# Performance work log

Measured on AMD Instinct MI355X. Metric: run time of the kernel, lower is better.

Reference implementation:

```python
import jax, jax.numpy as jnp
import numpy as np
from jax.scipy.special import logsumexp

NUM_TAGS = 128
B, S = 256, 1024


def setup_inputs() -> dict:
    key = jax.random.key(0)
    k1, k2, k3, k4, k5 = jax.random.split(key, 5)
    emissions = jax.random.normal(k1, (B, S, NUM_TAGS), dtype=jnp.float32)
    masks = jnp.ones((B, S), dtype=jnp.float32)
    tags = jax.random.randint(k2, (B, S), 0, NUM_TAGS, dtype=jnp.int64)
    transitions = jax.random.normal(k3, (NUM_TAGS, NUM_TAGS), dtype=jnp.float32)
    start_transitions = jax.random.normal(k4, (NUM_TAGS,), dtype=jnp.float32)
    end_transitions = jax.random.normal(k5, (NUM_TAGS,), dtype=jnp.float32)
    return {"emissions": emissions, "masks": masks, "tags": tags,
            "transitions": transitions, "start_transitions": start_transitions,
            "end_transitions": end_transitions}


def _crf_loss(emissions, masks, tags, transitions, start_transitions, end_transitions):
    b, s, t = emissions.shape

    # ---- forward algorithm (log partition) ----
    def step(alpha, xs):
        emit, m = xs  # emit: (B,T), m: (B,)
        # next[b,j] = logsumexp_i(alpha[b,i] + trans[i,j] + emit[b,j])
        nxt = logsumexp(alpha[:, :, None] + transitions[None, :, :] + emit[:, None, :], axis=1)
        alpha = jnp.where(m[:, None] > 0, nxt, alpha)
        return alpha, None

    alpha0 = jnp.broadcast_to(start_transitions[None, :], (b, t))
    # note: original torch code includes i=0 in the recurrence (applies transitions
    # from start_transitions into the first emission) -- replicated faithfully.
    alpha, _ = jax.lax.scan(step, alpha0,
                            (jnp.swapaxes(emissions, 0, 1), masks.T))
    log_z = logsumexp(alpha + end_transitions[None, :], axis=1)  # (B,)

    # ---- gold sequence score (vectorized over time) ----
    bidx = jnp.arange(b)
    score = start_transitions[tags[:, 0]]
    emit_g = jnp.take_along_axis(emissions, tags[:, :, None], axis=2)[..., 0]  # (B,S)
    score = score + jnp.sum(emit_g[:, : s - 1] * masks[:, : s - 1], axis=1)
    trans_g = transitions[tags[:, : s - 1], tags[:, 1:]]  # (B,S-1)
    score = score + jnp.sum(trans_g * masks[:, 1:], axis=1)
    last_ix = jnp.maximum(jnp.sum(masks, axis=1) - 1.0, 0.0).astype(jnp.int32)
    score = score + emissions[bidx, last_ix, tags[:, -1]] * masks[:, -1]
    score = score + end_transitions[tags[:, -1]] * masks[:, -1]

    return jnp.mean(log_z - score)


def reference(emissions, masks, tags, transitions, start_transitions, end_transitions):
    return _crf_loss(emissions, masks, tags, transitions, start_transitions, end_transitions)
```

## Files before the change

### kernel.cpp

```cpp
#include <hip/hip_runtime.h>

#define NT 128
#define SEQ 1024
#define NB 256

typedef _Float16 half2v __attribute__((ext_vector_type(2)));

#define DPP_MAX_STEP(x, ctrl)                                                   \
    fmaxf((x), __builtin_bit_cast(float, __builtin_amdgcn_update_dpp(           \
        __builtin_bit_cast(int, (x)), __builtin_bit_cast(int, (x)),             \
        (ctrl), 0xf, 0xf, false)))

__device__ __forceinline__ float wave_max_dpp(float x) {
    x = DPP_MAX_STEP(x, 0x111);
    x = DPP_MAX_STEP(x, 0x112);
    x = DPP_MAX_STEP(x, 0x114);
    x = DPP_MAX_STEP(x, 0x118);
    x = DPP_MAX_STEP(x, 0x142);
    x = DPP_MAX_STEP(x, 0x143);
    return __builtin_bit_cast(float, __builtin_amdgcn_readlane(
        __builtin_bit_cast(int, x), 63));
}

__device__ __forceinline__ float cross32_add(float x) {
    float a = x, b = x;
    asm volatile("v_permlane32_swap_b32 %0, %1" : "+v"(a), "+v"(b));
    return a + b;
}

__device__ __forceinline__ float swap1_dpp(float x) {
    return __builtin_bit_cast(float, __builtin_amdgcn_update_dpp(
        0, __builtin_bit_cast(int, x), 0xB1, 0xf, 0xf, true));
}

#define CRF_STEP(RC, RN, MC, DO_PRE, K, BUF)                                     \
    {                                                                            \
        float mcur = MC;                                                         \
        if (DO_PRE) { RC = emp[(K) * NT]; MC = mpp[K]; }                         \
        float eRN = __expf(RN);           \
        const uint4* p4 = (const uint4*)&p_lds[BUF][ih * 32];                    \
        float A0=0.f, A1=0.f, A2=0.f, A3=0.f;                                    \
        _Pragma("unroll")                                                        \
        for (int qi = 0; qi < 8; ++qi) {                                         \
            uint4 q = p4[qi];                                                    \
            A0 = __builtin_amdgcn_fdot2(__builtin_bit_cast(half2v, q.x),         \
                                        E[4*qi+0], A0, false);                   \
            A1 = __builtin_amdgcn_fdot2(__builtin_bit_cast(half2v, q.y),         \
                                        E[4*qi+1], A1, false);                   \
            A2 = __builtin_amdgcn_fdot2(__builtin_bit_cast(half2v, q.z),         \
                                        E[4*qi+2], A2, false);                   \
            A3 = __builtin_amdgcn_fdot2(__builtin_bit_cast(half2v, q.w),         \
                                        E[4*qi+3], A3, false);                   \
        }                                                                        \
        float sv = cross32_add((A0 + A1) + (A2 + A3));                           \
        float v = sv * ex;                                                       \
        if (mcur > 0.0f) { cur = v; offset += offadd; }                          \
        float curo = swap1_dpp(cur);            \
        if (ih == 0 && (cl & 1) == 0)                                            \
            p_lds[(BUF)^1][16*w + (cl >> 1)] = __builtin_bit_cast(unsigned int,  \
                __builtin_amdgcn_cvt_pkrtz(cur, curo));                          \
        float wm = wave_max_dpp(cur);                                            \
        if (l == 0) wmax[(BUF)^1][w] = wm;                                       \
        __syncthreads();                                                         \
        float4 wv = *(const float4*)&wmax[(BUF)^1][0];                           \
        mx = fmaxf(fmaxf(wv.x, wv.y), fmaxf(wv.z, wv.w));                        \
        inv = __builtin_amdgcn_rcpf(256.0f * mx);                                \
        offadd = __logf(mx) + 5.545177444479562f;                                \
        ex = eRN * inv;                                                          \
    }

__global__ __launch_bounds__(256, 1) void crf_scan_kernel(
    const float* __restrict__ emissions,
    const float* __restrict__ masks,
    const int*   __restrict__ tags,
    const float* __restrict__ transitions,
    const float* __restrict__ start_t,
    const float* __restrict__ end_t,
    float* __restrict__ out_per_batch)
{
    const int b   = blockIdx.x;
    const int tid = threadIdx.x;
    const int w   = tid >> 6;
    const int l   = tid & 63;
    const int cl  = l & 31;
    const int ih  = l >> 5;
    const int c   = 32 * w + cl;
    const int i0  = 64 * ih;

    __shared__ __align__(16) unsigned int p_lds[2][64];
    __shared__ __align__(16) float        wmax[2][4];
    __shared__ float redA[4], redB[4], redC[4];
    __shared__ float msk_s[SEQ];

    half2v E[32];
    #pragma unroll
    for (int r = 0; r < 32; ++r) {
        float ea = transitions[(i0 + 2*r    ) * NT + c];
        float ob = transitions[(i0 + 2*r + 1) * NT + c];
        E[r] = half2v{(_Float16)__expf(ea), (_Float16)__expf(ob)};
    }

    for (int s = tid; s < SEQ; s += 256)
        msk_s[s] = masks[b * SEQ + s];

    float cur = __expf(start_t[c]);
    float offset = 0.0f;

    {
        float curo = swap1_dpp(cur);
        if (ih == 0 && (cl & 1) == 0)
            p_lds[0][16*w + (cl >> 1)] = __builtin_bit_cast(unsigned int,
                __builtin_amdgcn_cvt_pkrtz(cur, curo));
        float wm = wave_max_dpp(cur);
        if (l == 0) wmax[0][w] = wm;
    }
    __syncthreads();

    float4 wv0 = *(const float4*)&wmax[0][0];
    float mx   = fmaxf(fmaxf(wv0.x, wv0.y), fmaxf(wv0.z, wv0.w));
    float inv  = __builtin_amdgcn_rcpf(256.0f * mx);
    float offadd = __logf(mx) + 5.545177444479562f;

    const float* eb  = emissions + (size_t)b * SEQ * NT;
    const float* mkp = masks + b * SEQ;

    float ring0 = eb[(size_t)0 * NT + c];
    float ring1 = eb[(size_t)1 * NT + c];
    float ring2 = eb[(size_t)2 * NT + c];
    float ring3 = eb[(size_t)3 * NT + c];
    float mr0 = mkp[0], mr1 = mkp[1], mr2 = mkp[2], mr3 = mkp[3];

    float ex = __expf(ring0) * inv;

    const float* emp = eb + 4 * NT + c;
    const float* mpp = mkp + 4;

    for (int it = 0; it < (SEQ - 4) / 4; ++it) {
        CRF_STEP(ring0, ring1, mr0, true, 0, 0)
        CRF_STEP(ring1, ring2, mr1, true, 1, 1)
        CRF_STEP(ring2, ring3, mr2, true, 2, 0)
        CRF_STEP(ring3, ring0, mr3, true, 3, 1)
        emp += 4 * NT;
        mpp += 4;
    }
    CRF_STEP(ring0, ring1, mr0, false, 0, 0)
    CRF_STEP(ring1, ring2, mr1, false, 0, 1)
    CRF_STEP(ring2, ring3, mr2, false, 0, 0)
    CRF_STEP(ring3, ring3, mr3, false, 0, 1)

    float term = (ih == 0) ? cur * __expf(end_t[c]) : 0.0f;
    #pragma unroll
    for (int off = 32; off; off >>= 1)
        term += __shfl_xor(term, off);
    if (l == 0) redA[w] = term;

    const int tbase = b * SEQ;
    float sc = 0.0f, sm = 0.0f;
    for (int s = tid; s < SEQ; s += 256) {
        float m = msk_s[s];
        sm += m;
        if (s < SEQ - 1) {
            int tg  = tags[tbase + s];
            int tg1 = tags[tbase + s + 1];
            sc += eb[(size_t)s * NT + tg] * m;
            sc += transitions[tg * NT + tg1] * msk_s[s + 1];
        }
    }
    #pragma unroll
    for (int off = 32; off; off >>= 1) {
        sc += __shfl_xor(sc, off);
        sm += __shfl_xor(sm, off);
    }
    if (l == 0) { redB[w] = sc; redC[w] = sm; }
    __syncthreads();

    if (tid == 0) {
        float term_t = (redA[0] + redA[1]) + (redA[2] + redA[3]);
        float log_z  = offset + __logf(term_t);
        float sct    = (redB[0] + redB[1]) + (redB[2] + redB[3]);
        float smt    = (redC[0] + redC[1]) + (redC[2] + redC[3]);
        int tg0 = tags[tbase];
        int tgl = tags[tbase + SEQ - 1];
        sct += start_t[tg0];
        int last_ix = (int)fmaxf(smt - 1.0f, 0.0f);
        float ml = msk_s[SEQ - 1];
        sct += eb[(size_t)last_ix * NT + tgl] * ml;
        sct += end_t[tgl] * ml;
        out_per_batch[b] = log_z - sct;
    }
}

__global__ void crf_reduce_kernel(const float* __restrict__ pb, float* __restrict__ out)
{
    float v = pb[threadIdx.x];
    #pragma unroll
    for (int off = 32; off; off >>= 1)
        v += __shfl_xor(v, off);
    __shared__ float s4[4];
    if ((threadIdx.x & 63) == 0) s4[threadIdx.x >> 6] = v;
    __syncthreads();
    if (threadIdx.x == 0)
        out[0] = (s4[0] + s4[1] + s4[2] + s4[3]) * (1.0f / 256.0f);
}

extern "C" void kernel_launch(void* const* d_in, const int* in_sizes, int n_in,
                              void* d_out, int out_size, void* d_ws, size_t ws_size,
                              hipStream_t stream) {
    const float* emissions   = (const float*)d_in[0];
    const float* masks       = (const float*)d_in[1];
    const int*   tags        = (const int*)  d_in[2];
    const float* transitions = (const float*)d_in[3];
    const float* start_t     = (const float*)d_in[4];
    const float* end_t       = (const float*)d_in[5];
    float* per_batch = (float*)d_ws;

    crf_scan_kernel<<<NB, 256, 0, stream>>>(emissions, masks, tags, transitions,
                                            start_t, end_t, per_batch);
    crf_reduce_kernel<<<1, 256, 0, stream>>>(per_batch, (float*)d_out);
}
```

Baseline: 558.4 us.

## Split CRF scan reduction over 512 threads with four-way lane partition

The block size doubles to 512 threads. Each lane now covers 32 source tags instead of 64, so it holds 16 packed exp-transition registers and runs 16 fdot2 per step instead of 32. Partial sums are combined with permlane16 and permlane32 swaps, and the per-wave max and final reductions are widened to 8 waves. The aim is to shorten the serial per-timestep dependency chain and put two waves on each SIMD to hide latency. In exchange, every step pays an extra cross-lane add and a barrier across 8 waves instead of 4.

```diff
diff --git a/kernel.cpp b/kernel.cpp
--- a/kernel.cpp
+++ b/kernel.cpp
@@ -28,6 +28,12 @@
     return a + b;
 }
 
+__device__ __forceinline__ float cross16_add(float x) {
+    float a = x, b = x;
+    asm volatile("v_permlane16_swap_b32 %0, %1" : "+v"(a), "+v"(b));
+    return a + b;
+}
+
 __device__ __forceinline__ float swap1_dpp(float x) {
     return __builtin_bit_cast(float, __builtin_amdgcn_update_dpp(
         0, __builtin_bit_cast(int, x), 0xB1, 0xf, 0xf, true));
@@ -38,10 +44,10 @@
         float mcur = MC;                                                         \
         if (DO_PRE) { RC = emp[(K) * NT]; MC = mpp[K]; }                         \
         float eRN = __expf(RN);           \
-        const uint4* p4 = (const uint4*)&p_lds[BUF][ih * 32];                    \
+        const uint4* p4 = (const uint4*)&p_lds[BUF][16 * kq];                    \
         float A0=0.f, A1=0.f, A2=0.f, A3=0.f;                                    \
         _Pragma("unroll")                                                        \
-        for (int qi = 0; qi < 8; ++qi) {                                         \
+        for (int qi = 0; qi < 4; ++qi) {                                         \
             uint4 q = p4[qi];                                                    \
             A0 = __builtin_amdgcn_fdot2(__builtin_bit_cast(half2v, q.x),         \
                                         E[4*qi+0], A0, false);                   \
@@ -52,24 +58,27 @@
             A3 = __builtin_amdgcn_fdot2(__builtin_bit_cast(half2v, q.w),         \
                                         E[4*qi+3], A3, false);                   \
         }                                                                        \
-        float sv = cross32_add((A0 + A1) + (A2 + A3));                           \
+        float part = (A0 + A1) + (A2 + A3);                                      \
+        float sv = cross32_add(cross16_add(part));                               \
         float v = sv * ex;                                                       \
         if (mcur > 0.0f) { cur = v; offset += offadd; }                          \
         float curo = swap1_dpp(cur);            \
-        if (ih == 0 && (cl & 1) == 0)                                            \
-            p_lds[(BUF)^1][16*w + (cl >> 1)] = __builtin_bit_cast(unsigned int,  \
+        if (kq == 0 && (cl & 1) == 0)                                            \
+            p_lds[(BUF)^1][8*w + (cl >> 1)] = __builtin_bit_cast(unsigned int,   \
                 __builtin_amdgcn_cvt_pkrtz(cur, curo));                          \
         float wm = wave_max_dpp(cur);                                            \
         if (l == 0) wmax[(BUF)^1][w] = wm;                                       \
         __syncthreads();                                                         \
-        float4 wv = *(const float4*)&wmax[(BUF)^1][0];                           \
-        mx = fmaxf(fmaxf(wv.x, wv.y), fmaxf(wv.z, wv.w));                        \
+        float4 wa = *(const float4*)&wmax[(BUF)^1][0];                           \
+        float4 wb = *(const float4*)&wmax[(BUF)^1][4];                           \
+        mx = fmaxf(fmaxf(fmaxf(wa.x, wa.y), fmaxf(wa.z, wa.w)),                  \
+                   fmaxf(fmaxf(wb.x, wb.y), fmaxf(wb.z, wb.w)));                 \
         inv = __builtin_amdgcn_rcpf(256.0f * mx);                                \
         offadd = __logf(mx) + 5.545177444479562f;                                \
         ex = eRN * inv;                                                          \
     }
 
-__global__ __launch_bounds__(256, 1) void crf_scan_kernel(
+__global__ __launch_bounds__(512, 1) void crf_scan_kernel(
     const float* __restrict__ emissions,
     const float* __restrict__ masks,
     const int*   __restrict__ tags,
@@ -82,25 +91,25 @@
     const int tid = threadIdx.x;
     const int w   = tid >> 6;
     const int l   = tid & 63;
-    const int cl  = l & 31;
-    const int ih  = l >> 5;
-    const int c   = 32 * w + cl;
-    const int i0  = 64 * ih;
+    const int cl  = l & 15;
+    const int kq  = l >> 4;
+    const int c   = 16 * w + cl;
+    const int i0  = 32 * kq;
 
     __shared__ __align__(16) unsigned int p_lds[2][64];
-    __shared__ __align__(16) float        wmax[2][4];
-    __shared__ float redA[4], redB[4], redC[4];
+    __shared__ __align__(16) float        wmax[2][8];
+    __shared__ float redA[8], redB[8], redC[8];
     __shared__ float msk_s[SEQ];
 
-    half2v E[32];
-    #pragma unroll
-    for (int r = 0; r < 32; ++r) {
-        float ea = transitions[(i0 + 2*r    ) * NT + c];
-        float ob = transitions[(i0 + 2*r + 1) * NT + c];
-        E[r] = half2v{(_Float16)__expf(ea), (_Float16)__expf(ob)};
-    }
-
-    for (int s = tid; s < SEQ; s += 256)
+    half2v E[16];
+    #pragma unroll
+    for (int u = 0; u < 16; ++u) {
+        float ea = transitions[(i0 + 2*u    ) * NT + c];
+        float ob = transitions[(i0 + 2*u + 1) * NT + c];
+        E[u] = half2v{(_Float16)__expf(ea), (_Float16)__expf(ob)};
+    }
+
+    for (int s = tid; s < SEQ; s += 512)
         msk_s[s] = masks[b * SEQ + s];
 
     float cur = __expf(start_t[c]);
@@ -108,16 +117,18 @@
 
     {
         float curo = swap1_dpp(cur);
-        if (ih == 0 && (cl & 1) == 0)
-            p_lds[0][16*w + (cl >> 1)] = __builtin_bit_cast(unsigned int,
+        if (kq == 0 && (cl & 1) == 0)
+            p_lds[0][8*w + (cl >> 1)] = __builtin_bit_cast(unsigned int,
                 __builtin_amdgcn_cvt_pkrtz(cur, curo));
         float wm = wave_max_dpp(cur);
         if (l == 0) wmax[0][w] = wm;
     }
     __syncthreads();
 
-    float4 wv0 = *(const float4*)&wmax[0][0];
-    float mx   = fmaxf(fmaxf(wv0.x, wv0.y), fmaxf(wv0.z, wv0.w));
+    float4 wa0 = *(const float4*)&wmax[0][0];
+    float4 wb0 = *(const float4*)&wmax[0][4];
+    float mx   = fmaxf(fmaxf(fmaxf(wa0.x, wa0.y), fmaxf(wa0.z, wa0.w)),
+                       fmaxf(fmaxf(wb0.x, wb0.y), fmaxf(wb0.z, wb0.w)));
     float inv  = __builtin_amdgcn_rcpf(256.0f * mx);
     float offadd = __logf(mx) + 5.545177444479562f;
 
@@ -148,7 +159,7 @@
     CRF_STEP(ring2, ring3, mr2, false, 0, 0)
     CRF_STEP(ring3, ring3, mr3, false, 0, 1)
 
-    float term = (ih == 0) ? cur * __expf(end_t[c]) : 0.0f;
+    float term = (kq == 0) ? cur * __expf(end_t[c]) : 0.0f;
     #pragma unroll
     for (int off = 32; off; off >>= 1)
         term += __shfl_xor(term, off);
@@ -156,7 +167,7 @@
 
     const int tbase = b * SEQ;
     float sc = 0.0f, sm = 0.0f;
-    for (int s = tid; s < SEQ; s += 256) {
+    for (int s = tid; s < SEQ; s += 512) {
         float m = msk_s[s];
         sm += m;
         if (s < SEQ - 1) {
@@ -175,10 +186,13 @@
     __syncthreads();
 
     if (tid == 0) {
-        float term_t = (redA[0] + redA[1]) + (redA[2] + redA[3]);
+        float term_t = ((redA[0] + redA[1]) + (redA[2] + redA[3]))
+                     + ((redA[4] + redA[5]) + (redA[6] + redA[7]));
         float log_z  = offset + __logf(term_t);
-        float sct    = (redB[0] + redB[1]) + (redB[2] + redB[3]);
-        float smt    = (redC[0] + redC[1]) + (redC[2] + redC[3]);
+        float sct    = ((redB[0] + redB[1]) + (redB[2] + redB[3]))
+                     + ((redB[4] + redB[5]) + (redB[6] + redB[7]));
+        float smt    = ((redC[0] + redC[1]) + (redC[2] + redC[3]))
+                     + ((redC[4] + redC[5]) + (redC[6] + redC[7]));
         int tg0 = tags[tbase];
         int tgl = tags[tbase + SEQ - 1];
         sct += start_t[tg0];
@@ -214,7 +228,7 @@
     const float* end_t       = (const float*)d_in[5];
     float* per_batch = (float*)d_ws;
 
-    crf_scan_kernel<<<NB, 256, 0, stream>>>(emissions, masks, tags, transitions,
+    crf_scan_kernel<<<NB, 512, 0, stream>>>(emissions, masks, tags, transitions,
                                             start_t, end_t, per_batch);
     crf_reduce_kernel<<<1, 256, 0, stream>>>(per_batch, (float*)d_out);
 }
```

Measured after the change: 628.0 us. 1.12x slower.

## Remap threads to two columns per lane and compute scaling max from shared probabilities

Applied to the files above, without the earlier changes.

Each lane now owns two output tags and a quarter of the source tags (k split into 4 groups of 32), reducing via permlane16 and permlane32 swaps. The per-step scaling max is no longer published through a separate shared wmax array. Each wave instead recomputes it from the packed half probabilities it already reads from LDS, using packed f16 max and a DPP wave reduction. This removes one LDS round trip and shortens the serial dependency after the barrier. The cost is some redundant max work per wave and extra cross-lane reduction steps.

```diff
diff --git a/kernel.cpp b/kernel.cpp
--- a/kernel.cpp
+++ b/kernel.cpp
@@ -28,45 +28,79 @@
     return a + b;
 }
 
-__device__ __forceinline__ float swap1_dpp(float x) {
-    return __builtin_bit_cast(float, __builtin_amdgcn_update_dpp(
-        0, __builtin_bit_cast(int, x), 0xB1, 0xf, 0xf, true));
-}
-
-#define CRF_STEP(RC, RN, MC, DO_PRE, K, BUF)                                     \
+__device__ __forceinline__ float cross16_add(float x) {
+    float a = x, b = x;
+    asm volatile("v_permlane16_swap_b32 %0, %1" : "+v"(a), "+v"(b));
+    return a + b;
+}
+
+__device__ __forceinline__ unsigned int pk_max_u(unsigned int a, unsigned int b) {
+    unsigned int r;
+    asm("v_pk_max_f16 %0, %1, %2" : "=v"(r) : "v"(a), "v"(b));
+    return r;
+}
+
+#define CRF_STEP(RC, MC, DO_PRE, K, BUF)                                         \
     {                                                                            \
+        float2 emv = RC;                                                         \
         float mcur = MC;                                                         \
-        if (DO_PRE) { RC = emp[(K) * NT]; MC = mpp[K]; }                         \
-        float eRN = __expf(RN);           \
-        const uint4* p4 = (const uint4*)&p_lds[BUF][ih * 32];                    \
-        float A0=0.f, A1=0.f, A2=0.f, A3=0.f;                                    \
-        _Pragma("unroll")                                                        \
-        for (int qi = 0; qi < 8; ++qi) {                                         \
-            uint4 q = p4[qi];                                                    \
-            A0 = __builtin_amdgcn_fdot2(__builtin_bit_cast(half2v, q.x),         \
-                                        E[4*qi+0], A0, false);                   \
-            A1 = __builtin_amdgcn_fdot2(__builtin_bit_cast(half2v, q.y),         \
-                                        E[4*qi+1], A1, false);                   \
-            A2 = __builtin_amdgcn_fdot2(__builtin_bit_cast(half2v, q.z),         \
-                                        E[4*qi+2], A2, false);                   \
-            A3 = __builtin_amdgcn_fdot2(__builtin_bit_cast(half2v, q.w),         \
-                                        E[4*qi+3], A3, false);                   \
-        }                                                                        \
-        float sv = cross32_add((A0 + A1) + (A2 + A3));                           \
-        float v = sv * ex;                                                       \
-        if (mcur > 0.0f) { cur = v; offset += offadd; }                          \
-        float curo = swap1_dpp(cur);            \
-        if (ih == 0 && (cl & 1) == 0)                                            \
-            p_lds[(BUF)^1][16*w + (cl >> 1)] = __builtin_bit_cast(unsigned int,  \
-                __builtin_amdgcn_cvt_pkrtz(cur, curo));                          \
-        float wm = wave_max_dpp(cur);                                            \
-        if (l == 0) wmax[(BUF)^1][w] = wm;                                       \
+        if (DO_PRE) { RC = *(const float2*)(emp + (K) * NT); MC = mpp[K]; }      \
+        float e2x = __expf(emv.x), e2y = __expf(emv.y);                          \
+        const uint4* p4 = (const uint4*)&p_lds[BUF][16 * kq];                    \
+        uint4 q0 = p4[0], q1 = p4[1], q2 = p4[2], q3 = p4[3];                    \
+              \
+        unsigned int m0 = pk_max_u(pk_max_u(q0.x, q0.y), pk_max_u(q0.z, q0.w));  \
+        unsigned int m1 = pk_max_u(pk_max_u(q1.x, q1.y), pk_max_u(q1.z, q1.w));  \
+        unsigned int m2 = pk_max_u(pk_max_u(q2.x, q2.y), pk_max_u(q2.z, q2.w));  \
+        unsigned int m3 = pk_max_u(pk_max_u(q3.x, q3.y), pk_max_u(q3.z, q3.w));  \
+        unsigned int mm = pk_max_u(pk_max_u(m0, m1), pk_max_u(m2, m3));          \
+        half2v mh = __builtin_bit_cast(half2v, mm);                              \
+        float mx = wave_max_dpp(fmaxf((float)mh.x, (float)mh.y));                \
+        float inv = __builtin_amdgcn_rcpf(256.0f * mx);                          \
+        float offadd = __logf(mx) + 5.545177444479562f;                          \
+        float ex0 = e2x * inv, ex1 = e2y * inv;                                  \
+        float A0=0.f,A1=0.f,A2=0.f,A3=0.f,B0=0.f,B1=0.f,B2=0.f,B3=0.f;           \
+        A0 = __builtin_amdgcn_fdot2(__builtin_bit_cast(half2v,q0.x), E0[0],  A0, false); \
+        B0 = __builtin_amdgcn_fdot2(__builtin_bit_cast(half2v,q0.x), E1[0],  B0, false); \
+        A1 = __builtin_amdgcn_fdot2(__builtin_bit_cast(half2v,q0.y), E0[1],  A1, false); \
+        B1 = __builtin_amdgcn_fdot2(__builtin_bit_cast(half2v,q0.y), E1[1],  B1, false); \
+        A2 = __builtin_amdgcn_fdot2(__builtin_bit_cast(half2v,q0.z), E0[2],  A2, false); \
+        B2 = __builtin_amdgcn_fdot2(__builtin_bit_cast(half2v,q0.z), E1[2],  B2, false); \
+        A3 = __builtin_amdgcn_fdot2(__builtin_bit_cast(half2v,q0.w), E0[3],  A3, false); \
+        B3 = __builtin_amdgcn_fdot2(__builtin_bit_cast(half2v,q0.w), E1[3],  B3, false); \
+        A0 = __builtin_amdgcn_fdot2(__builtin_bit_cast(half2v,q1.x), E0[4],  A0, false); \
+        B0 = __builtin_amdgcn_fdot2(__builtin_bit_cast(half2v,q1.x), E1[4],  B0, false); \
+        A1 = __builtin_amdgcn_fdot2(__builtin_bit_cast(half2v,q1.y), E0[5],  A1, false); \
+        B1 = __builtin_amdgcn_fdot2(__builtin_bit_cast(half2v,q1.y), E1[5],  B1, false); \
+        A2 = __builtin_amdgcn_fdot2(__builtin_bit_cast(half2v,q1.z), E0[6],  A2, false); \
+        B2 = __builtin_amdgcn_fdot2(__builtin_bit_cast(half2v,q1.z), E1[6],  B2, false); \
+        A3 = __builtin_amdgcn_fdot2(__builtin_bit_cast(half2v,q1.w), E0[7],  A3, false); \
+        B3 = __builtin_amdgcn_fdot2(__builtin_bit_cast(half2v,q1.w), E1[7],  B3, false); \
+        A0 = __builtin_amdgcn_fdot2(__builtin_bit_cast(half2v,q2.x), E0[8],  A0, false); \
+        B0 = __builtin_amdgcn_fdot2(__builtin_bit_cast(half2v,q2.x), E1[8],  B0, false); \
+        A1 = __builtin_amdgcn_fdot2(__builtin_bit_cast(half2v,q2.y), E0[9],  A1, false); \
+        B1 = __builtin_amdgcn_fdot2(__builtin_bit_cast(half2v,q2.y), E1[9],  B1, false); \
+        A2 = __builtin_amdgcn_fdot2(__builtin_bit_cast(half2v,q2.z), E0[10], A2, false); \
+        B2 = __builtin_amdgcn_fdot2(__builtin_bit_cast(half2v,q2.z), E1[10], B2, false); \
+        A3 = __builtin_amdgcn_fdot2(__builtin_bit_cast(half2v,q2.w), E0[11], A3, false); \
+        B3 = __builtin_amdgcn_fdot2(__builtin_bit_cast(half2v,q2.w), E1[11], B3, false); \
+        A0 = __builtin_amdgcn_fdot2(__builtin_bit_cast(half2v,q3.x), E0[12], A0, false); \
+        B0 = __builtin_amdgcn_fdot2(__builtin_bit_cast(half2v,q3.x), E1[12], B0, false); \
+        A1 = __builtin_amdgcn_fdot2(__builtin_bit_cast(half2v,q3.y), E0[13], A1, false); \
+        B1 = __builtin_amdgcn_fdot2(__builtin_bit_cast(half2v,q3.y), E1[13], B1, false); \
+        A2 = __builtin_amdgcn_fdot2(__builtin_bit_cast(half2v,q3.z), E0[14], A2, false); \
+        B2 = __builtin_amdgcn_fdot2(__builtin_bit_cast(half2v,q3.z), E1[14], B2, false); \
+        A3 = __builtin_amdgcn_fdot2(__builtin_bit_cast(half2v,q3.w), E0[15], A3, false); \
+        B3 = __builtin_amdgcn_fdot2(__builtin_bit_cast(half2v,q3.w), E1[15], B3, false); \
+        float sA = cross32_add(cross16_add((A0 + A1) + (A2 + A3)));              \
+        float sB = cross32_add(cross16_add((B0 + B1) + (B2 + B3)));              \
+        float v0 = sA * ex0;                                                     \
+        float v1 = sB * ex1;                                                     \
+        if (mcur > 0.0f) { cur0 = v0; cur1 = v1; offset += offadd; }             \
+        if (kq == 0)                                                             \
+            p_lds[(BUF)^1][16*w + cl] = __builtin_bit_cast(unsigned int,         \
+                __builtin_amdgcn_cvt_pkrtz(cur0, cur1));                         \
         __syncthreads();                                                         \
-        float4 wv = *(const float4*)&wmax[(BUF)^1][0];                           \
-        mx = fmaxf(fmaxf(wv.x, wv.y), fmaxf(wv.z, wv.w));                        \
-        inv = __builtin_amdgcn_rcpf(256.0f * mx);                                \
-        offadd = __logf(mx) + 5.545177444479562f;                                \
-        ex = eRN * inv;                                                          \
     }
 
 __global__ __launch_bounds__(256, 1) void crf_scan_kernel(
@@ -82,73 +116,64 @@
     const int tid = threadIdx.x;
     const int w   = tid >> 6;
     const int l   = tid & 63;
-    const int cl  = l & 31;
-    const int ih  = l >> 5;
-    const int c   = 32 * w + cl;
-    const int i0  = 64 * ih;
+    const int cl  = l & 15;
+    const int kq  = l >> 4;
+    const int c0  = 32 * w + 2 * cl;
+    const int c1  = c0 + 1;
+    const int i0  = 32 * kq;
 
     __shared__ __align__(16) unsigned int p_lds[2][64];
-    __shared__ __align__(16) float        wmax[2][4];
     __shared__ float redA[4], redB[4], redC[4];
     __shared__ float msk_s[SEQ];
 
-    half2v E[32];
-    #pragma unroll
-    for (int r = 0; r < 32; ++r) {
-        float ea = transitions[(i0 + 2*r    ) * NT + c];
-        float ob = transitions[(i0 + 2*r + 1) * NT + c];
-        E[r] = half2v{(_Float16)__expf(ea), (_Float16)__expf(ob)};
+    half2v E0[16], E1[16];
+    #pragma unroll
+    for (int j = 0; j < 16; ++j) {
+        float2 ta = *(const float2*)&transitions[(i0 + 2*j    ) * NT + c0];
+        float2 tb = *(const float2*)&transitions[(i0 + 2*j + 1) * NT + c0];
+        E0[j] = half2v{(_Float16)__expf(ta.x), (_Float16)__expf(tb.x)};
+        E1[j] = half2v{(_Float16)__expf(ta.y), (_Float16)__expf(tb.y)};
     }
 
     for (int s = tid; s < SEQ; s += 256)
         msk_s[s] = masks[b * SEQ + s];
 
-    float cur = __expf(start_t[c]);
+    float cur0 = __expf(start_t[c0]);
+    float cur1 = __expf(start_t[c1]);
     float offset = 0.0f;
 
-    {
-        float curo = swap1_dpp(cur);
-        if (ih == 0 && (cl & 1) == 0)
-            p_lds[0][16*w + (cl >> 1)] = __builtin_bit_cast(unsigned int,
-                __builtin_amdgcn_cvt_pkrtz(cur, curo));
-        float wm = wave_max_dpp(cur);
-        if (l == 0) wmax[0][w] = wm;
-    }
+    if (kq == 0)
+        p_lds[0][16*w + cl] = __builtin_bit_cast(unsigned int,
+            __builtin_amdgcn_cvt_pkrtz(cur0, cur1));
     __syncthreads();
-
-    float4 wv0 = *(const float4*)&wmax[0][0];
-    float mx   = fmaxf(fmaxf(wv0.x, wv0.y), fmaxf(wv0.z, wv0.w));
-    float inv  = __builtin_amdgcn_rcpf(256.0f * mx);
-    float offadd = __logf(mx) + 5.545177444479562f;
 
     const float* eb  = emissions + (size_t)b * SEQ * NT;
     const float* mkp = masks + b * SEQ;
 
-    float ring0 = eb[(size_t)0 * NT + c];
-    float ring1 = eb[(size_t)1 * NT + c];
-    float ring2 = eb[(size_t)2 * NT + c];
-    float ring3 = eb[(size_t)3 * NT + c];
-    float mr0 = mkp[0], mr1 = mkp[1], mr2 = mkp[2], mr3 = mkp[3];
-
-    float ex = __expf(ring0) * inv;
-
-    const float* emp = eb + 4 * NT + c;
+    float2 ring0 = *(const float2*)&eb[(size_t)0 * NT + c0];
+    float2 ring1 = *(const float2*)&eb[(size_t)1 * NT + c0];
+    float2 ring2 = *(const float2*)&eb[(size_t)2 * NT + c0];
+    float2 ring3 = *(const float2*)&eb[(size_t)3 * NT + c0];
+    float  mr0 = mkp[0], mr1 = mkp[1], mr2 = mkp[2], mr3 = mkp[3];
+
+    const float* emp = eb + 4 * NT + c0;
     const float* mpp = mkp + 4;
 
     for (int it = 0; it < (SEQ - 4) / 4; ++it) {
-        CRF_STEP(ring0, ring1, mr0, true, 0, 0)
-        CRF_STEP(ring1, ring2, mr1, true, 1, 1)
-        CRF_STEP(ring2, ring3, mr2, true, 2, 0)
-        CRF_STEP(ring3, ring0, mr3, true, 3, 1)
+        CRF_STEP(ring0, mr0, true, 0, 0)
+        CRF_STEP(ring1, mr1, true, 1, 1)
+        CRF_STEP(ring2, mr2, true, 2, 0)
+        CRF_STEP(ring3, mr3, true, 3, 1)
         emp += 4 * NT;
         mpp += 4;
     }
-    CRF_STEP(ring0, ring1, mr0, false, 0, 0)
-    CRF_STEP(ring1, ring2, mr1, false, 0, 1)
-    CRF_STEP(ring2, ring3, mr2, false, 0, 0)
-    CRF_STEP(ring3, ring3, mr3, false, 0, 1)
-
-    float term = (ih == 0) ? cur * __expf(end_t[c]) : 0.0f;
+    CRF_STEP(ring0, mr0, false, 0, 0)
+    CRF_STEP(ring1, mr1, false, 0, 1)
+    CRF_STEP(ring2, mr2, false, 0, 0)
+    CRF_STEP(ring3, mr3, false, 0, 1)
+
+    float term = (kq == 0)
+               ? cur0 * __expf(end_t[c0]) + cur1 * __expf(end_t[c1]) : 0.0f;
     #pragma unroll
     for (int off = 32; off; off >>= 1)
         term += __shfl_xor(term, off);
```

New measurement: 620.9 us. 11.2% more time.

## Batch CRF forward recursion over 16 sequences with MFMA and pre-exponentiated emissions

Applied to the files above, without the earlier changes.

Replaces the per-batch 256-thread scan, which does fdot2 work and a block barrier every step, with a single-wave MFMA scan. Each wave handles 16 batch rows and does the 128x128 matrix-vector product as 16x16x32 f16 MFMAs, with the max reduction done by permlane swaps instead of LDS plus __syncthreads. Emissions are exponentiated and packed to fp16 in a separate prepass kernel, and the gold-score computation moves to its own kernel. Only 16 workgroups run the serial scan, so the GPU is heavily underused. It also adds a workspace-size-dependent fallback and more fp16 rounding.

```diff
diff --git a/kernel.cpp b/kernel.cpp
--- a/kernel.cpp
+++ b/kernel.cpp
@@ -3,8 +3,12 @@
 #define NT 128
 #define SEQ 1024
 #define NB 256
+#define NBLK 16
 
 typedef _Float16 half2v __attribute__((ext_vector_type(2)));
+typedef _Float16 half8  __attribute__((ext_vector_type(8)));
+typedef float    f32x4  __attribute__((ext_vector_type(4)));
+
 
 #define DPP_MAX_STEP(x, ctrl)                                                   \
     fmaxf((x), __builtin_bit_cast(float, __builtin_amdgcn_update_dpp(           \
@@ -27,38 +31,309 @@
     asm volatile("v_permlane32_swap_b32 %0, %1" : "+v"(a), "+v"(b));
     return a + b;
 }
-
+__device__ __forceinline__ float cross16_add(float x) {
+    float a = x, b = x;
+    asm volatile("v_permlane16_swap_b32 %0, %1" : "+v"(a), "+v"(b));
+    return a + b;
+}
+__device__ __forceinline__ float cross32_max(float x) {
+    float a = x, b = x;
+    asm volatile("v_permlane32_swap_b32 %0, %1" : "+v"(a), "+v"(b));
+    return fmaxf(a, b);
+}
+__device__ __forceinline__ float cross16_max(float x) {
+    float a = x, b = x;
+    asm volatile("v_permlane16_swap_b32 %0, %1" : "+v"(a), "+v"(b));
+    return fmaxf(a, b);
+}
 __device__ __forceinline__ float swap1_dpp(float x) {
     return __builtin_bit_cast(float, __builtin_amdgcn_update_dpp(
         0, __builtin_bit_cast(int, x), 0xB1, 0xf, 0xf, true));
 }
 
-#define CRF_STEP(RC, RN, MC, DO_PRE, K, BUF)                                     \
+__device__ __forceinline__ unsigned int pkrtz_u(float a, float b) {
+    return __builtin_bit_cast(unsigned int, __builtin_amdgcn_cvt_pkrtz(a, b));
+}
+__device__ __forceinline__ f32x4 mfma16(uint4 a, uint4 b, f32x4 c) {
+    return __builtin_amdgcn_mfma_f32_16x16x32_f16(
+        __builtin_bit_cast(half8, a), __builtin_bit_cast(half8, b), c, 0, 0, 0);
+}
+__device__ __forceinline__ unsigned int packexp2(const float* p, int i0, int i1) {
+    half2v h;
+    h.x = (_Float16)__expf(p[i0]);
+    h.y = (_Float16)__expf(p[i1]);
+    return __builtin_bit_cast(unsigned int, h);
+}
+
+__global__ void crf_preexp_kernel(const float* __restrict__ em,
+                                  unsigned int* __restrict__ X) {
+    const unsigned int total = (unsigned int)NB * SEQ * 64u;
+    for (unsigned int o = blockIdx.x * blockDim.x + threadIdx.x; o < total;
+         o += gridDim.x * blockDim.x) {
+        const unsigned int bs  = o >> 6;
+        const unsigned int w6  = o & 63u;
+        const unsigned int lg_ = w6 >> 4;
+        const unsigned int t_  = (w6 >> 1) & 7u;
+        const unsigned int i_  = w6 & 1u;
+        const unsigned int tag = 16u * t_ + 4u * lg_ + 2u * i_;
+        const float2 e = *(const float2*)&em[(size_t)bs * NT + tag];
+        half2v h;
+        h.x = (_Float16)__expf(e.x);
+        h.y = (_Float16)__expf(e.y);
+        X[o] = __builtin_bit_cast(unsigned int, h);
+    }
+}
+
+__global__ __launch_bounds__(256, 1) void crf_score_kernel(
+    const float* __restrict__ emissions, const float* __restrict__ masks,
+    const int* __restrict__ tags, const float* __restrict__ transitions,
+    const float* __restrict__ start_t, const float* __restrict__ end_t,
+    float* __restrict__ score_pb)
+{
+    const int b = blockIdx.x, tid = threadIdx.x;
+    const int w = tid >> 6, l = tid & 63;
+    __shared__ float msk_s[SEQ];
+    __shared__ float redB[4], redC[4];
+    for (int s = tid; s < SEQ; s += 256)
+        msk_s[s] = masks[b * SEQ + s];
+    __syncthreads();
+    const float* eb = emissions + (size_t)b * SEQ * NT;
+    const int tbase = b * SEQ;
+    float sc = 0.0f, sm = 0.0f;
+    for (int s = tid; s < SEQ; s += 256) {
+        const float m = msk_s[s];
+        sm += m;
+        if (s < SEQ - 1) {
+            const int tg  = tags[tbase + s];
+            const int tg1 = tags[tbase + s + 1];
+            sc += eb[(size_t)s * NT + tg] * m;
+            sc += transitions[tg * NT + tg1] * msk_s[s + 1];
+        }
+    }
+    #pragma unroll
+    for (int off = 32; off; off >>= 1) {
+        sc += __shfl_xor(sc, off);
+        sm += __shfl_xor(sm, off);
+    }
+    if (l == 0) { redB[w] = sc; redC[w] = sm; }
+    __syncthreads();
+    if (tid == 0) {
+        float sct = (redB[0] + redB[1]) + (redB[2] + redB[3]);
+        float smt = (redC[0] + redC[1]) + (redC[2] + redC[3]);
+        const int tg0 = tags[tbase];
+        const int tgl = tags[tbase + SEQ - 1];
+        sct += start_t[tg0];
+        const int last_ix = (int)fmaxf(smt - 1.0f, 0.0f);
+        const float ml = msk_s[SEQ - 1];
+        sct += eb[(size_t)last_ix * NT + tgl] * ml;
+        sct += end_t[tgl] * ml;
+        score_pb[b] = sct;
+    }
+}
+
+
+#define TILEPAIR(PK, RJ, CA, CB)                                                 \
+    {                                                                            \
+        const half2v h0_ = __builtin_bit_cast(half2v, RJ.x);                     \
+        const half2v h1_ = __builtin_bit_cast(half2v, RJ.y);                     \
+        const half2v h2_ = __builtin_bit_cast(half2v, RJ.z);                     \
+        const half2v h3_ = __builtin_bit_cast(half2v, RJ.w);                     \
+        const float v0_ = CA[0] * ((float)h0_.x * inv);                          \
+        const float v1_ = CA[1] * ((float)h0_.y * inv);                          \
+        const float v2_ = CA[2] * ((float)h1_.x * inv);                          \
+        const float v3_ = CA[3] * ((float)h1_.y * inv);                          \
+        const float v4_ = CB[0] * ((float)h2_.x * inv);                          \
+        const float v5_ = CB[1] * ((float)h2_.y * inv);                          \
+        const float v6_ = CB[2] * ((float)h3_.x * inv);                          \
+        const float v7_ = CB[3] * ((float)h3_.y * inv);                          \
+        PK.x = sel_ ? pkrtz_u(v0_, v1_) : PK.x;                                  \
+        PK.y = sel_ ? pkrtz_u(v2_, v3_) : PK.y;                                  \
+        PK.z = sel_ ? pkrtz_u(v4_, v5_) : PK.z;                                  \
+        PK.w = sel_ ? pkrtz_u(v6_, v7_) : PK.w;                                  \
+        tmax_ = fmaxf(tmax_, fmaxf(fmaxf(v0_, v1_), fmaxf(v2_, v3_)));           \
+        tmax_ = fmaxf(tmax_, fmaxf(fmaxf(v4_, v5_), fmaxf(v6_, v7_)));           \
+    }
+
+#define SCAN_STEP(R0, R1, R2, R3, MV, MPRE, DO_PRE, POFF, MOFF)                  \
+    {                                                                            \
+        const float m_ = MV;                                                     \
+        const bool sel_ = (m_ > 0.0f);                                           \
+        f32x4 C[8];                                                              \
+        _Pragma("unroll")                                                        \
+        for (int t = 0; t < 8; ++t) { C[t][0]=0.f; C[t][1]=0.f; C[t][2]=0.f; C[t][3]=0.f; } \
+        _Pragma("unroll")                                                        \
+        for (int t = 0; t < 8; ++t) C[t] = mfma16(Af[t][0], pkA, C[t]);          \
+        _Pragma("unroll")                                                        \
+        for (int t = 0; t < 8; ++t) C[t] = mfma16(Af[t][1], pkB, C[t]);          \
+        _Pragma("unroll")                                                        \
+        for (int t = 0; t < 8; ++t) C[t] = mfma16(Af[t][2], pkC, C[t]);          \
+        _Pragma("unroll")                                                        \
+        for (int t = 0; t < 8; ++t) C[t] = mfma16(Af[t][3], pkD, C[t]);          \
+        float tmax_ = -3.4e38f;                                                  \
+        TILEPAIR(pkA, R0, C[0], C[1])                                            \
+        TILEPAIR(pkB, R1, C[2], C[3])                                            \
+        TILEPAIR(pkC, R2, C[4], C[5])                                            \
+        TILEPAIR(pkD, R3, C[6], C[7])                                            \
+        offset += sel_ ? offadd : 0.0f;                                          \
+        const float am_ = cross32_max(cross16_max(tmax_));                       \
+        mx = sel_ ? am_ : mx;                                                    \
+        inv = __builtin_amdgcn_rcpf(256.0f * mx);                                \
+        offadd = __logf(mx) + 5.545177444479562f;                                \
+        if (DO_PRE) {                                                            \
+            R0 = *(const uint4*)(xp + (POFF));                                   \
+            R1 = *(const uint4*)(xp + (POFF) + 4);                               \
+            R2 = *(const uint4*)(xp + (POFF) + 8);                               \
+            R3 = *(const uint4*)(xp + (POFF) + 12);                              \
+            MPRE = mp[MOFF];                                                     \
+        }                                                                        \
+    }
+
+#define INITQ(PK, J)                                                             \
+    {                                                                            \
+        const int tb0 = 16 * (2 * (J)) + 4 * lg, tb1 = tb0 + 16;                 \
+        const float a0 = __expf(start_t[tb0 + 0]), a1 = __expf(start_t[tb0 + 1]);\
+        const float a2 = __expf(start_t[tb0 + 2]), a3 = __expf(start_t[tb0 + 3]);\
+        const float b0 = __expf(start_t[tb1 + 0]), b1 = __expf(start_t[tb1 + 1]);\
+        const float b2 = __expf(start_t[tb1 + 2]), b3 = __expf(start_t[tb1 + 3]);\
+        PK.x = pkrtz_u(a0, a1); PK.y = pkrtz_u(a2, a3);                          \
+        PK.z = pkrtz_u(b0, b1); PK.w = pkrtz_u(b2, b3);                          \
+        tmax0 = fmaxf(tmax0, fmaxf(fmaxf(a0, a1), fmaxf(a2, a3)));               \
+        tmax0 = fmaxf(tmax0, fmaxf(fmaxf(b0, b1), fmaxf(b2, b3)));               \
+    }
+
+#define TERMQ(PK, J)                                                             \
+    {                                                                            \
+        const half2v h0_ = __builtin_bit_cast(half2v, PK.x);                     \
+        const half2v h1_ = __builtin_bit_cast(half2v, PK.y);                     \
+        const half2v h2_ = __builtin_bit_cast(half2v, PK.z);                     \
+        const half2v h3_ = __builtin_bit_cast(half2v, PK.w);                     \
+        const int t0_ = 16 * (2 * (J)) + 4 * lg, t1_ = t0_ + 16;                 \
+        eterm += (float)h0_.x * __expf(end_t[t0_ + 0]);                          \
+        eterm += (float)h0_.y * __expf(end_t[t0_ + 1]);                          \
+        eterm += (float)h1_.x * __expf(end_t[t0_ + 2]);                          \
+        eterm += (float)h1_.y * __expf(end_t[t0_ + 3]);                          \
+        eterm += (float)h2_.x * __expf(end_t[t1_ + 0]);                          \
+        eterm += (float)h2_.y * __expf(end_t[t1_ + 1]);                          \
+        eterm += (float)h3_.x * __expf(end_t[t1_ + 2]);                          \
+        eterm += (float)h3_.y * __expf(end_t[t1_ + 3]);                          \
+    }
+
+__global__ __launch_bounds__(64, 1) void crf_mfma_scan_kernel(
+    const unsigned int* __restrict__ X,
+    const float* __restrict__ masks,
+    const float* __restrict__ transitions,
+    const float* __restrict__ start_t,
+    const float* __restrict__ end_t,
+    float* __restrict__ logz_pb)
+{
+    const int li  = threadIdx.x & 15;
+    const int lg  = threadIdx.x >> 4;
+    const int b16 = blockIdx.x * 16;
+
+    uint4 Af[8][4];
+    #pragma unroll
+    for (int t = 0; t < 8; ++t) {
+        const int col = 16 * t + li;
+        #pragma unroll
+        for (int kc = 0; kc < 4; ++kc) {
+            const int kb = 32 * kc + 4 * lg;
+            uint4 q;
+            q.x = packexp2(transitions, (kb + 0)  * NT + col, (kb + 1)  * NT + col);
+            q.y = packexp2(transitions, (kb + 2)  * NT + col, (kb + 3)  * NT + col);
+            q.z = packexp2(transitions, (kb + 16) * NT + col, (kb + 17) * NT + col);
+            q.w = packexp2(transitions, (kb + 18) * NT + col, (kb + 19) * NT + col);
+            Af[t][kc] = q;
+        }
+    }
+
+    uint4 pkA, pkB, pkC, pkD;
+    float tmax0 = -3.4e38f;
+    INITQ(pkA, 0) INITQ(pkB, 1) INITQ(pkC, 2) INITQ(pkD, 3)
+    float mx = cross32_max(cross16_max(tmax0));
+    float inv = __builtin_amdgcn_rcpf(256.0f * mx);
+    float offadd = __logf(mx) + 5.545177444479562f;
+    float offset = 0.0f;
+
+    const unsigned int* xp = X + ((size_t)(b16 + li) * SEQ) * 64 + lg * 16;
+    const float* mp = masks + (size_t)(b16 + li) * SEQ;
+    uint4 Ra0 = *(const uint4*)(xp + 0),  Ra1 = *(const uint4*)(xp + 4);
+    uint4 Ra2 = *(const uint4*)(xp + 8),  Ra3 = *(const uint4*)(xp + 12);
+    uint4 Rb0 = *(const uint4*)(xp + 64), Rb1 = *(const uint4*)(xp + 68);
+    uint4 Rb2 = *(const uint4*)(xp + 72), Rb3 = *(const uint4*)(xp + 76);
+    float mA = mp[0], mB = mp[1];
+
+    for (int it = 0; it < (SEQ - 2) / 2; ++it) {
+        SCAN_STEP(Ra0, Ra1, Ra2, Ra3, mA, mA, true, 128, 2)
+        SCAN_STEP(Rb0, Rb1, Rb2, Rb3, mB, mB, true, 192, 3)
+        xp += 128;
+        mp += 2;
+    }
+    SCAN_STEP(Ra0, Ra1, Ra2, Ra3, mA, mA, false, 0, 0)
+    SCAN_STEP(Rb0, Rb1, Rb2, Rb3, mB, mB, false, 0, 0)
+
+    float eterm = 0.0f;
+    TERMQ(pkA, 0) TERMQ(pkB, 1) TERMQ(pkC, 2) TERMQ(pkD, 3)
+    eterm = cross32_add(cross16_add(eterm));
+    const float log_z = offset + __logf(eterm);
+    if (lg == 0)
+        logz_pb[b16 + li] = log_z;
+}
+
+__global__ void crf_reduce2_kernel(const float* __restrict__ logz,
+                                   const float* __restrict__ score,
+                                   float* __restrict__ out)
+{
+    float v = logz[threadIdx.x] - score[threadIdx.x];
+    #pragma unroll
+    for (int off = 32; off; off >>= 1)
+        v += __shfl_xor(v, off);
+    __shared__ float s4[4];
+    if ((threadIdx.x & 63) == 0) s4[threadIdx.x >> 6] = v;
+    __syncthreads();
+    if (threadIdx.x == 0)
+        out[0] = (s4[0] + s4[1] + s4[2] + s4[3]) * (1.0f / 256.0f);
+}
+
+__global__ void crf_reduce_kernel(const float* __restrict__ pb, float* __restrict__ out)
+{
+    float v = pb[threadIdx.x];
+    #pragma unroll
+    for (int off = 32; off; off >>= 1)
+        v += __shfl_xor(v, off);
+    __shared__ float s4[4];
+    if ((threadIdx.x & 63) == 0) s4[threadIdx.x >> 6] = v;
+    __syncthreads();
+    if (threadIdx.x == 0)
+        out[0] = (s4[0] + s4[1] + s4[2] + s4[3]) * (1.0f / 256.0f);
+}
+
+typedef _Float16 half2f __attribute__((ext_vector_type(2)));
+
+#define CRF_STEP_FB(RC, RN, MC, DO_PRE, K, BUF)                                  \
     {                                                                            \
         float mcur = MC;                                                         \
         if (DO_PRE) { RC = emp[(K) * NT]; MC = mpp[K]; }                         \
-        float eRN = __expf(RN);           \
+        float eRN = __expf(RN);                                                  \
         const uint4* p4 = (const uint4*)&p_lds[BUF][ih * 32];                    \
         float A0=0.f, A1=0.f, A2=0.f, A3=0.f;                                    \
         _Pragma("unroll")                                                        \
         for (int qi = 0; qi < 8; ++qi) {                                         \
             uint4 q = p4[qi];                                                    \
-            A0 = __builtin_amdgcn_fdot2(__builtin_bit_cast(half2v, q.x),         \
+            A0 = __builtin_amdgcn_fdot2(__builtin_bit_cast(half2f, q.x),         \
                                         E[4*qi+0], A0, false);                   \
-            A1 = __builtin_amdgcn_fdot2(__builtin_bit_cast(half2v, q.y),         \
+            A1 = __builtin_amdgcn_fdot2(__builtin_bit_cast(half2f, q.y),         \
                                         E[4*qi+1], A1, false);                   \
-            A2 = __builtin_amdgcn_fdot2(__builtin_bit_cast(half2v, q.z),         \
+            A2 = __builtin_amdgcn_fdot2(__builtin_bit_cast(half2f, q.z),         \
                                         E[4*qi+2], A2, false);                   \
-            A3 = __builtin_amdgcn_fdot2(__builtin_bit_cast(half2v, q.w),         \
+            A3 = __builtin_amdgcn_fdot2(__builtin_bit_cast(half2f, q.w),         \
                                         E[4*qi+3], A3, false);                   \
         }                                                                        \
         float sv = cross32_add((A0 + A1) + (A2 + A3));                           \
         float v = sv * ex;                                                       \
         if (mcur > 0.0f) { cur = v; offset += offadd; }                          \
-        float curo = swap1_dpp(cur);            \
+        float curo = swap1_dpp(cur);                                             \
         if (ih == 0 && (cl & 1) == 0)                                            \
-            p_lds[(BUF)^1][16*w + (cl >> 1)] = __builtin_bit_cast(unsigned int,  \
-                __builtin_amdgcn_cvt_pkrtz(cur, curo));                          \
+            p_lds[(BUF)^1][16*w + (cl >> 1)] = pkrtz_u(cur, curo);               \
         float wm = wave_max_dpp(cur);                                            \
         if (l == 0) wmax[(BUF)^1][w] = wm;                                       \
         __syncthreads();                                                         \
@@ -69,13 +344,10 @@
         ex = eRN * inv;                                                          \
     }
 
-__global__ __launch_bounds__(256, 1) void crf_scan_kernel(
-    const float* __restrict__ emissions,
-    const float* __restrict__ masks,
-    const int*   __restrict__ tags,
-    const float* __restrict__ transitions,
-    const float* __restrict__ start_t,
-    const float* __restrict__ end_t,
+__global__ __launch_bounds__(256, 1) void crf_scan_fallback(
+    const float* __restrict__ emissions, const float* __restrict__ masks,
+    const int* __restrict__ tags, const float* __restrict__ transitions,
+    const float* __restrict__ start_t, const float* __restrict__ end_t,
     float* __restrict__ out_per_batch)
 {
     const int b   = blockIdx.x;
@@ -92,25 +364,22 @@
     __shared__ float redA[4], redB[4], redC[4];
     __shared__ float msk_s[SEQ];
 
-    half2v E[32];
+    half2f E[32];
     #pragma unroll
     for (int r = 0; r < 32; ++r) {
         float ea = transitions[(i0 + 2*r    ) * NT + c];
         float ob = transitions[(i0 + 2*r + 1) * NT + c];
-        E[r] = half2v{(_Float16)__expf(ea), (_Float16)__expf(ob)};
-    }
-
+        E[r] = half2f{(_Float16)__expf(ea), (_Float16)__expf(ob)};
+    }
     for (int s = tid; s < SEQ; s += 256)
         msk_s[s] = masks[b * SEQ + s];
 
     float cur = __expf(start_t[c]);
     float offset = 0.0f;
-
     {
         float curo = swap1_dpp(cur);
         if (ih == 0 && (cl & 1) == 0)
-            p_lds[0][16*w + (cl >> 1)] = __builtin_bit_cast(unsigned int,
-                __builtin_amdgcn_cvt_pkrtz(cur, curo));
+            p_lds[0][16*w + (cl >> 1)] = pkrtz_u(cur, curo);
         float wm = wave_max_dpp(cur);
         if (l == 0) wmax[0][w] = wm;
     }
@@ -123,30 +392,27 @@
 
     const float* eb  = emissions + (size_t)b * SEQ * NT;
     const float* mkp = masks + b * SEQ;
-
     float ring0 = eb[(size_t)0 * NT + c];
     float ring1 = eb[(size_t)1 * NT + c];
     float ring2 = eb[(size_t)2 * NT + c];
     float ring3 = eb[(size_t)3 * NT + c];
     float mr0 = mkp[0], mr1 = mkp[1], mr2 = mkp[2], mr3 = mkp[3];
-
     float ex = __expf(ring0) * inv;
-
     const float* emp = eb + 4 * NT + c;
     const float* mpp = mkp + 4;
 
     for (int it = 0; it < (SEQ - 4) / 4; ++it) {
-        CRF_STEP(ring0, ring1, mr0, true, 0, 0)
-        CRF_STEP(ring1, ring2, mr1, true, 1, 1)
-        CRF_STEP(ring2, ring3, mr2, true, 2, 0)
-        CRF_STEP(ring3, ring0, mr3, true, 3, 1)
+        CRF_STEP_FB(ring0, ring1, mr0, true, 0, 0)
+        CRF_STEP_FB(ring1, ring2, mr1, true, 1, 1)
+        CRF_STEP_FB(ring2, ring3, mr2, true, 2, 0)
+        CRF_STEP_FB(ring3, ring0, mr3, true, 3, 1)
         emp += 4 * NT;
         mpp += 4;
     }
-    CRF_STEP(ring0, ring1, mr0, false, 0, 0)
-    CRF_STEP(ring1, ring2, mr1, false, 0, 1)
-    CRF_STEP(ring2, ring3, mr2, false, 0, 0)
-    CRF_STEP(ring3, ring3, mr3, false, 0, 1)
+    CRF_STEP_FB(ring0, ring1, mr0, false, 0, 0)
+    CRF_STEP_FB(ring1, ring2, mr1, false, 0, 1)
+    CRF_STEP_FB(ring2, ring3, mr2, false, 0, 0)
+    CRF_STEP_FB(ring3, ring3, mr3, false, 0, 1)
 
     float term = (ih == 0) ? cur * __expf(end_t[c]) : 0.0f;
     #pragma unroll
@@ -190,19 +456,6 @@
     }
 }
 
-__global__ void crf_reduce_kernel(const float* __restrict__ pb, float* __restrict__ out)
-{
-    float v = pb[threadIdx.x];
-    #pragma unroll
-    for (int off = 32; off; off >>= 1)
-        v += __shfl_xor(v, off);
-    __shared__ float s4[4];
-    if ((threadIdx.x & 63) == 0) s4[threadIdx.x >> 6] = v;
-    __syncthreads();
-    if (threadIdx.x == 0)
-        out[0] = (s4[0] + s4[1] + s4[2] + s4[3]) * (1.0f / 256.0f);
-}
-
 extern "C" void kernel_launch(void* const* d_in, const int* in_sizes, int n_in,
                               void* d_out, int out_size, void* d_ws, size_t ws_size,
                               hipStream_t stream) {
@@ -212,9 +465,22 @@
     const float* transitions = (const float*)d_in[3];
     const float* start_t     = (const float*)d_in[4];
     const float* end_t       = (const float*)d_in[5];
-    float* per_batch = (float*)d_ws;
-
-    crf_scan_kernel<<<NB, 256, 0, stream>>>(emissions, masks, tags, transitions,
-                                            start_t, end_t, per_batch);
-    crf_reduce_kernel<<<1, 256, 0, stream>>>(per_batch, (float*)d_out);
-}
+
+    const size_t X_BYTES = (size_t)NB * SEQ * 64 * 4;
+    if (ws_size >= X_BYTES + 4096) {
+        float* logz_pb  = (float*)d_ws;
+        float* score_pb = logz_pb + 256;
+        unsigned int* X = (unsigned int*)((char*)d_ws + 4096);
+        crf_preexp_kernel<<<2048, 256, 0, stream>>>(emissions, X);
+        crf_score_kernel<<<NB, 256, 0, stream>>>(emissions, masks, tags,
+                                                 transitions, start_t, end_t, score_pb);
+        crf_mfma_scan_kernel<<<NBLK, 64, 0, stream>>>(X, masks, transitions,
+                                                      start_t, end_t, logz_pb);
+        crf_reduce2_kernel<<<1, 256, 0, stream>>>(logz_pb, score_pb, (float*)d_out);
+    } else {
+        float* per_batch = (float*)d_ws;
+        crf_scan_fallback<<<NB, 256, 0, stream>>>(emissions, masks, tags,
+                                                  transitions, start_t, end_t, per_batch);
+        crf_reduce_kernel<<<1, 256, 0, stream>>>(per_batch, (float*)d_out);
+    }
+}
```

Measured after the change: 898.6 us. 1.61x slower.
